# Optimization experiments

Hardware: AMD Instinct MI355X
Metric: run time of the kernel (lower is better)

Reference implementation:

```python
import jax, jax.numpy as jnp
import numpy as np

SR = 22050
L = 2097153            # output_size = int(SR*95.109); equals NFFT//2+1 so spectral broadcast is well-defined
NFFT = 4194304         # 2**ceil(log2(L))
BANDS = [(1.0, 4.0), (4.0, 8.0), (8.0, 13.0), (13.0, 30.0), (30.0, 100.0), (100.0, 200.0)]
SPEC = [7.83, 528.0, 396.0, 2.5, 14.1, 432.0, 6.0, 30.0]
WIN = 15               # min(15, NFFT//100)
FREQS_NP = np.fft.rfftfreq(NFFT, 1.0 / SR).astype(np.float32)
FREQS = jnp.asarray(FREQS_NP)


def _freq_mod(sig, band_w, freq_w, harm_prog, tm_w1, tm_b1, tm_w2, tm_b2, tm_w3, tm_b3):
    t = jnp.arange(L, dtype=jnp.float32)
    Xf = jnp.fft.rfft(jnp.pad(sig, (0, NFFT - L)))            # [L] complex64
    # sequential band enhancements == product of per-band multipliers
    mult = jnp.ones((L,), jnp.float32)
    for b, (lo, hi) in enumerate(BANDS):
        c = (lo + hi) / 2.0
        w = (hi - lo) / 2.0
        mask = jnp.exp(-0.5 * ((FREQS - c) / (w / 2.0)) ** 2)
        mask = jnp.where((FREQS < lo) | (FREQS > hi), 0.0, mask)
        tmod = jnp.sin(2.0 * np.pi * c * t / SR)
        mult = mult * (1.0 + mask * band_w[b] * (1.0 + 0.2 * tmod))
    # harmonic progression (identical for every specific frequency -> compute once)
    tn = (t / L)[:, None]
    h = jax.nn.relu(tn @ tm_w1 + tm_b1)
    h = jax.nn.relu(h @ tm_w2 + tm_b2)
    mp = h @ tm_w3 + tm_b3                                    # [L, 8]
    chord_idx = jnp.floor(t / L * 8.0).astype(jnp.int32) % 8
    chord = harm_prog[chord_idx] * (1.0 + mp[:, 1] * jnp.sin(2.0 * np.pi * t / L))[:, None]
    prog_mean = chord.mean()
    # specific-frequency harmonic windows (static indices; commutative multiplies)
    smult = jnp.ones((L,), jnp.float32)
    for k, f in enumerate(SPEC):
        for m in (1.0, 2.0, 3.0, 4.0, 5.0):
            hf = f * m
            if hf >= SR / 2:
                continue
            hidx = int(np.argmin(np.abs(FREQS_NP - hf)))
            s = max(0, hidx - WIN)
            e = min(L - 1, hidx + WIN)
            win = jnp.asarray(np.exp(-0.5 * ((np.arange(s, e + 1) - hidx) / (WIN / 3.0)) ** 2).astype(np.float32))
            enh = freq_w[k] * win * (1.0 / m ** 1.2) * (1.0 + prog_mean)
            smult = smult.at[s:e + 1].multiply(1.0 + enh)
    Xf = Xf * mult * smult
    mag = jnp.abs(Xf)
    ph = jnp.angle(Xf)
    mag_s = jnp.concatenate([mag[:1], mag[1:-1] * 0.7 + mag[:-2] * 0.15 + mag[2:] * 0.15, mag[-1:]])
    Xc = mag_s * jnp.exp(1j * ph)
    return jnp.fft.irfft(Xc, n=NFFT)[:L]


def _conv1d(x, w, b, stride):
    y = jax.lax.conv_general_dilated(x, w, (stride,), [(2, 2)], dimension_numbers=("NCH", "OIH", "NCH"))
    return y + b[None, :, None]


def setup_inputs() -> dict:
    key = jax.random.key(0)
    ks = jax.random.split(key, 16)
    n = lambda k, s, sc=1.0: jax.random.normal(k, s, dtype=jnp.float32) * sc
    return {
        "z": n(ks[0], (1, 1, L)),
        "condition": n(ks[1], (1, 8)),
        "band_w": jnp.full((6,), 0.5, jnp.float32),
        "freq_w": jnp.full((8,), 0.3, jnp.float32),
        "harm_prog": n(ks[2], (8, 4)),
        "tm_w1": n(ks[3], (1, 32), 0.5), "tm_b1": jnp.zeros((32,), jnp.float32),
        "tm_w2": n(ks[4], (32, 16), 0.2), "tm_b2": jnp.zeros((16,), jnp.float32),
        "tm_w3": n(ks[5], (16, 8), 0.2), "tm_b3": jnp.zeros((8,), jnp.float32),
        "c1_w": n(ks[6], (32, 1, 5), 0.3), "c1_b": jnp.zeros((32,), jnp.float32),
        "c2_w": n(ks[7], (64, 32, 5), 0.08), "c2_b": jnp.zeros((64,), jnp.float32),
        "c3_w": n(ks[8], (128, 64, 5), 0.05), "c3_b": jnp.zeros((128,), jnp.float32),
        "mx_w1": n(ks[9], (192, 256), 0.07), "mx_b1": jnp.zeros((256,), jnp.float32),
        "mx_w2": n(ks[10], (256, 1), 0.06), "mx_b2": jnp.zeros((1,), jnp.float32),
    }


def reference(z, condition, band_w, freq_w, harm_prog, tm_w1, tm_b1, tm_w2, tm_b2, tm_w3, tm_b3,
              c1_w, c1_b, c2_w, c2_b, c3_w, c3_b, mx_w1, mx_b1, mx_w2, mx_b2):
    base = _freq_mod(z[0, 0], band_w, freq_w, harm_prog, tm_w1, tm_b1, tm_w2, tm_b2, tm_w3, tm_b3)[None, None, :]
    h = jax.nn.leaky_relu(_conv1d(base, c1_w, c1_b, 2), 0.2)
    h = jax.nn.leaky_relu(_conv1d(h, c2_w, c2_b, 2), 0.2)
    h = jax.nn.leaky_relu(_conv1d(h, c3_w, c3_b, 2), 0.2)
    feat = h.mean(axis=2)                                     # [1, 128]
    emb = jnp.zeros((1, 64), jnp.float32)                     # instrument_idx=None path
    mixed = jnp.concatenate([feat, emb], axis=1)              # [1, 192]
    out = jax.nn.leaky_relu(mixed @ mx_w1 + mx_b1, 0.2) @ mx_w2 + mx_b2
    return out
```

## Files before the change

kernel.cpp:

```cpp
#include <hip/hip_runtime.h>
#include <cmath>

#define LSIG  2097153
#define MH    2097152
#define NFFTC 4194304
#define NT128 16384
#define O1C   1048577
#define O2C   524289
#define O3C   262145

#define TO3   62
#define NB3   4229

#define A_OFF    0
#define B_OFF    16777216
#define PM_OFF   58720268
#define FEAT_OFF 58720272
#define W2Q_OFF  50331664
#define W3Q_OFF  50352144
#define W1Q_OFF  50434064

struct SmultTab { int hidx[40]; float inv12[40]; int fk[40]; int maxe; };

typedef short short8 __attribute__((ext_vector_type(8)));
typedef float f32x4v __attribute__((ext_vector_type(4)));

union AFrag { uint4 q; short8 s; };
union BFrag { uint4 q; unsigned int u[4]; short8 s; };

__device__ __forceinline__ float lrelu(float a){ return a > 0.0f ? a : 0.2f*a; }

__device__ __forceinline__ float hsin(float rev){ return __builtin_amdgcn_sinf(rev); }
__device__ __forceinline__ float hcos(float rev){ return __builtin_amdgcn_cosf(rev); }

__device__ __forceinline__ unsigned int rbf(float f) {
  unsigned int u = __float_as_uint(f);
  u += 0x7fffu + ((u >> 16) & 1u);
  return u >> 16;
}
__device__ __forceinline__ unsigned int pack_bf2(float a, float b) {
  unsigned int r;
  asm("v_cvt_pk_bf16_f32 %0, %1, %2" : "=v"(r) : "v"(a), "v"(b));
  return r;
}

__device__ __forceinline__ int swz1(int pos, int dw) {
  return (pos*16 + dw) ^ (((pos >> 1) & 7) << 2);
}
__device__ __forceinline__ int swz2(int pos, int dw) {
  return (pos*32 + dw) ^ (((pos >> 1) & 7) << 2);
}

__device__ __forceinline__ int slot128(int jj, int q) {
  int s = q ^ ((q >> 4) & 7);
  return jj*128 + ((s + 9*jj) & 127);
}

__device__ __forceinline__ float2 cadd(float2 a, float2 b){ return make_float2(a.x+b.x, a.y+b.y); }
__device__ __forceinline__ float2 csub(float2 a, float2 b){ return make_float2(a.x-b.x, a.y-b.y); }

template<bool FWD> __device__ __forceinline__ float2 jrot(float2 z){
  return FWD ? make_float2(z.y, -z.x) : make_float2(-z.y, z.x);
}

template<bool FWD> __device__ __forceinline__ void dft8(float2 v[8]) {
  const float cq = 0.70710678118654752440f;
  const float S  = FWD ? -1.0f : 1.0f;
  float2 e0 = cadd(v[0], v[4]), e1 = csub(v[0], v[4]);
  float2 e2 = cadd(v[2], v[6]), e3 = csub(v[2], v[6]);
  float2 E0 = cadd(e0, e2), E2 = csub(e0, e2);
  float2 jt = jrot<FWD>(e3);
  float2 E1 = cadd(e1, jt), E3 = csub(e1, jt);
  float2 o0 = cadd(v[1], v[5]), o1 = csub(v[1], v[5]);
  float2 o2 = cadd(v[3], v[7]), o3 = csub(v[3], v[7]);
  float2 O0 = cadd(o0, o2), O2 = csub(o0, o2);
  float2 jo = jrot<FWD>(o3);
  float2 O1 = cadd(o1, jo), O3 = csub(o1, jo);
  float2 w1 = make_float2(cq*O1.x - S*cq*O1.y, cq*O1.y + S*cq*O1.x);
  float2 w2 = jrot<FWD>(O2);
  float2 w3 = make_float2(-cq*O3.x - S*cq*O3.y, -cq*O3.y + S*cq*O3.x);
  v[0] = cadd(E0, O0); v[4] = csub(E0, O0);
  v[1] = cadd(E1, w1); v[5] = csub(E1, w1);
  v[2] = cadd(E2, w2); v[6] = csub(E2, w2);
  v[3] = cadd(E3, w3); v[7] = csub(E3, w3);
}

template<bool FWD>
__device__ __forceinline__ void fft128_body(float2* stage, int t, int jb, int Ns) {
  const float ssg = FWD ? -1.0f : 1.0f;
  const float invden = 1.0f / (float)(128 * Ns);
  {
    const int jj = t >> 4, b = t & 15;
    const int m = (jb + jj) & (Ns - 1);
    float2 v[8];
#pragma unroll
    for (int a = 0; a < 8; ++a) {
      const int r = 16*a + b;
      float2 x = stage[slot128(jj, r)];
      if (Ns > 1) {
        float rev = (float)(m * r) * invden;
        float sn = ssg * hsin(rev), cs = hcos(rev);
        x = make_float2(x.x*cs - x.y*sn, x.x*sn + x.y*cs);
      }
      v[a] = x;
    }
    dft8<FWD>(v);
#pragma unroll
    for (int d = 0; d < 8; ++d)
      stage[slot128(jj, 16*d + b)] = v[d];
  }
  __syncthreads();
  {
    float2 y[16];
    const int jj = (t & 255) >> 3, d = t & 7;
    if (t < 256) {
#pragma unroll
      for (int b = 0; b < 16; ++b) {
        float2 x = stage[slot128(jj, 16*d + b)];
        float rev = (float)(b*d) * 0.0078125f;
        float sn = ssg * hsin(rev), cs = hcos(rev);
        y[b] = make_float2(x.x*cs - x.y*sn, x.x*sn + x.y*cs);
      }
    }
    __syncthreads();
    if (t < 256) {
      float2 E[8], O[8];
#pragma unroll
      for (int b = 0; b < 8; ++b) { E[b] = y[2*b]; O[b] = y[2*b+1]; }
      dft8<FWD>(E);
      dft8<FWD>(O);
#pragma unroll
      for (int c = 0; c < 8; ++c) {
        float rev = (float)c * 0.0625f;
        float sn = ssg * hsin(rev), cs = hcos(rev);
        float2 To = make_float2(O[c].x*cs - O[c].y*sn, O[c].x*sn + O[c].y*cs);
        stage[slot128(jj, 8*c + d)]      = cadd(E[c], To);
        stage[slot128(jj, 8*c + 64 + d)] = csub(E[c], To);
      }
    }
  }
  __syncthreads();
}

template<bool FWD, bool TRUNC>
__global__ __launch_bounds__(512) void kfft128(const float2* __restrict__ src,
                                               float2* __restrict__ dst, int Ns) {
  __shared__ float2 stage[4096];
  const int t = threadIdx.x;
  const int jb = blockIdx.x * 32;
  for (int c = 0; c < 4; ++c) {
    int u = t + 512*c;
    int jp = u & 15, rr = u >> 4;
    float4 q = *(const float4*)&src[jb + 2*jp + rr*NT128];
    stage[slot128(2*jp,   rr)] = make_float2(q.x, q.y);
    stage[slot128(2*jp+1, rr)] = make_float2(q.z, q.w);
  }
  __syncthreads();
  fft128_body<FWD>(stage, t, jb, Ns);
  if (Ns == 1) {
    for (int c = 0; c < 4; ++c) {
      int u = t + 512*c;
      int jj = u >> 6, k2 = (u & 63) * 2;
      float2 a = stage[slot128(jj, k2)], b = stage[slot128(jj, k2+1)];
      *(float4*)&dst[(jb + jj)*128 + k2] = make_float4(a.x, a.y, b.x, b.y);
    }
  } else {
    for (int c = 0; c < 4; ++c) {
      int u = t + 512*c;
      int pi = u & 15, k = u >> 4;
      int jj = 2*pi, j2 = jb + jj, m2 = j2 & (Ns - 1);
      int base = (j2 - m2)*128 + m2 + k*Ns;
      if (TRUNC && k >= 64) {
        if (k == 64 && j2 == 0) dst[base] = stage[slot128(jj, k)];
        continue;
      }
      float2 a = stage[slot128(jj, k)], b = stage[slot128(jj+1, k)];
      *(float4*)&dst[base] = make_float4(a.x, a.y, b.x, b.y);
    }
  }
}

__global__ __launch_bounds__(512) void kfirst(
    const float* __restrict__ zin, float2* __restrict__ dst,
    const float* __restrict__ tw1, const float* __restrict__ tb1,
    const float* __restrict__ tw2, const float* __restrict__ tb2,
    const float* __restrict__ tw3, const float* __restrict__ tb3,
    const float* __restrict__ hp, float* __restrict__ pm,
    float* __restrict__ feat) {
  __shared__ float2 stage[4096];
  __shared__ float shp[8];
  __shared__ float red[512];
  const int t = threadIdx.x;
  const int bb = blockIdx.x;
  if (bb < 512) {
    const int jb = bb * 32;
    for (int c = 0; c < 4; ++c) {
      int u = t + 512*c;
      int jp = u & 15, rr = u >> 4;
      int n = jb + 2*jp + rr*NT128;
      float2 a0, a1;
      if (n < 1048576) {
        float4 q = *(const float4*)&((const float2*)zin)[n];
        a0 = make_float2(q.x, q.y); a1 = make_float2(q.z, q.w);
      } else if (n == 1048576) {
        a0 = make_float2(zin[2097152], 0.0f); a1 = make_float2(0.0f, 0.0f);
      } else {
        a0 = make_float2(0.0f, 0.0f); a1 = a0;
      }
      stage[slot128(2*jp,   rr)] = a0;
      stage[slot128(2*jp+1, rr)] = a1;
    }
    __syncthreads();
    fft128_body<true>(stage, t, jb, 1);
    for (int c = 0; c < 4; ++c) {
      int u = t + 512*c;
      int jj = u >> 6, k2 = (u & 63) * 2;
      float2 a = stage[slot128(jj, k2)], b = stage[slot128(jj, k2+1)];
      *(float4*)&dst[(jb + jj)*128 + k2] = make_float4(a.x, a.y, b.x, b.y);
    }
    return;
  }
  if (t < 8) { float s = 0.f; for (int j = 0; j < 4; ++j) s += hp[t*4+j]; shp[t] = s; }
  __syncthreads();
  const int gid = (bb - 512)*512 + t;
  if (gid < 32768) feat[gid] = 0.0f;
  const float Lf = 2097153.0f;
  float tnv[4], sv[4];
  int ci[4];
  float acc[4][16];
#pragma unroll
  for (int e = 0; e < 4; ++e) {
    float ti = (float)(gid + e*524288);
    float tn = ti / Lf;
    tnv[e] = tn;
    sv[e] = hsin(tn);
    ci[e] = ((int)floorf(tn * 8.0f)) & 7;
#pragma unroll
    for (int kk = 0; kk < 16; ++kk) acc[e][kk] = tb2[kk];
  }
  for (int j = 0; j < 32; ++j) {
    float a = tw1[j], b = tb1[j];
    float hj[4];
#pragma unroll
    for (int e = 0; e < 4; ++e) hj[e] = fmaxf(a*tnv[e] + b, 0.0f);
#pragma unroll
    for (int kk = 0; kk < 16; ++kk) {
      float w = tw2[j*16 + kk];
#pragma unroll
      for (int e = 0; e < 4; ++e) acc[e][kk] += hj[e]*w;
    }
  }
  float lsum = 0.0f;
  const float b31 = tb3[1];
#pragma unroll
  for (int e = 0; e < 4; ++e) {
    float mp1 = b31;
#pragma unroll
    for (int kk = 0; kk < 16; ++kk) mp1 += fmaxf(acc[e][kk], 0.0f)*tw3[kk*8+1];
    lsum += shp[ci[e]] * (1.0f + mp1*sv[e]);
  }
  if (gid == 0) {
    float ti = 2097152.0f;
    float tn = ti / Lf;
    float a1[16];
    for (int kk = 0; kk < 16; ++kk) a1[kk] = tb2[kk];
    for (int j = 0; j < 32; ++j) {
      float h = fmaxf(tw1[j]*tn + tb1[j], 0.0f);
      for (int kk = 0; kk < 16; ++kk) a1[kk] += h*tw2[j*16+kk];
    }
    float mp1 = b31;
    for (int kk = 0; kk < 16; ++kk) mp1 += fmaxf(a1[kk], 0.0f)*tw3[kk*8+1];
    float svx = hsin(tn);
    int cix = ((int)floorf(tn * 8.0f)) & 7;
    lsum += shp[cix] * (1.0f + mp1*svx);
  }
  red[t] = lsum;
  __syncthreads();
  for (int off = 256; off > 0; off >>= 1) {
    if (t < off) red[t] += red[t+off];
    __syncthreads();
  }
  if (t == 0) atomicAdd(pm, red[0]);
}

__device__ __forceinline__ float2 xsplit(float2 zk, float2 zm, float rev) {
  float2 s  = make_float2(zk.x + zm.x, zk.y - zm.y);
  float2 dd = make_float2(zk.x - zm.x, zk.y + zm.y);
  float sn = -hsin(rev), cs = hcos(rev);
  float2 t1 = make_float2(cs*dd.x - sn*dd.y, cs*dd.y + sn*dd.x);
  return make_float2(0.5f*(s.x + t1.y), 0.5f*(s.y - t1.x));
}
__device__ __forceinline__ float2 scale_xc(float2 c, float mg, float ms) {
  if (mg > 0.0f) { float sc = ms/mg; return make_float2(c.x*sc, c.y*sc); }
  return make_float2(ms, 0.0f);
}
__device__ __forceinline__ float2 invpack(int n, float2 a, float2 b) {
  float2 s  = make_float2(a.x + b.x, a.y - b.y);
  float2 dd = make_float2(a.x - b.x, a.y + b.y);
  float rev = (float)n * (1.0f / (float)NFFTC);
  float sn = hsin(rev), cs = hcos(rev);
  float2 xo = make_float2(0.5f*(cs*dd.x - sn*dd.y), 0.5f*(cs*dd.y + sn*dd.x));
  const float sc = 1.0f / (float)MH;
  return make_float2((0.5f*s.x - xo.y)*sc, (0.5f*s.y + xo.x)*sc);
}

__global__ __launch_bounds__(256) void kspectral(const float2* __restrict__ Z,
    float2* __restrict__ A, const float* __restrict__ bwp,
    const float* __restrict__ fwp, const float* __restrict__ pm_in, SmultTab tab,
    const float* __restrict__ c1w, const float* __restrict__ c2w,
    const float* __restrict__ c3w, unsigned short* __restrict__ w1q,
    unsigned short* __restrict__ w2q, unsigned short* __restrict__ w3q) {
  const int bb = blockIdx.x;
  const int t = threadIdx.x;
  if (bb >= 4096) {
    int i = (bb - 4096)*256 + t;
    if (i < 1024) {
      int e = i & 7, u4 = i >> 3;
      int col = u4 & 15, quad = (u4 >> 4) & 3, mi = u4 >> 6;
      float v = (quad == 0 && e < 5) ? c1w[(mi*16 + col)*5 + e] : 0.0f;
      w1q[i] = (unsigned short)rbf(v);
    }
    if (i < 10240) {
      int e = i & 7, u4 = i >> 3;
      int col = u4 & 15, quad = (u4 >> 4) & 3, mtkt = u4 >> 6;
      int kt = mtkt % 5, mt = mtkt / 5;
      int ch = mt*16 + col, c1 = quad*8 + e;
      w2q[i] = (unsigned short)rbf(c2w[ch*160 + c1*5 + kt]);
    }
    if (i < 40960) {
      int e = i & 7, u4 = i >> 3;
      int col = u4 & 15, quad = (u4 >> 4) & 3, mtkt = u4 >> 6;
      int kt = mtkt % 10, mt = mtkt / 10;
      int ch = mt*16 + col, c2 = (kt & 1)*32 + quad*8 + e;
      w3q[i] = (unsigned short)rbf(c3w[ch*320 + c2*5 + (kt >> 1)]);
    }
    return;
  }
  __shared__ float2 Xlo[258], Xhi[258];
  __shared__ float  Mlo[258], Mhi[258];
  const int k0 = bb * 256;
  const float pm1 = 1.0f + pm_in[0] * (1.0f/8388612.0f);
  for (int w = t; w < 258; w += 256) {
    int k = k0 - 1 + w;
    float2 zk = Z[k & (MH-1)];
    float2 zm = Z[(MH - k) & (MH-1)];
    {
      float2 X = xsplit(zk, zm, (float)k * (1.0f/(float)NFFTC));
      float mv = 1.0f;
      if (k <= 38050) {
        const float blo[6] = {1.0f,4.0f,8.0f,13.0f,30.0f,100.0f};
        const float bhi[6] = {4.0f,8.0f,13.0f,30.0f,100.0f,200.0f};
        const float bcn[6] = {2.5f,6.0f,10.5f,21.5f,65.0f,150.0f};
        const float bhw[6] = {0.75f,1.0f,1.25f,4.25f,17.5f,25.0f};
        float f = (float)((double)k * (22050.0/4194304.0));
#pragma unroll
        for (int b = 0; b < 6; ++b) {
          if (f >= blo[b] && f <= bhi[b]) {
            float q = (f - bcn[b]) / bhw[b];
            float mask = expf(-0.5f*q*q);
            double frd = (double)k * ((double)bcn[b] / 22050.0);
            frd -= floor(frd);
            float tm = hsin((float)frd);
            mv *= (1.0f + mask * bwp[b] * (1.0f + 0.2f*tm));
          }
        }
      }
      if (k <= tab.maxe) {
        for (int ww = 0; ww < 40; ++ww) {
          int dlt = k - tab.hidx[ww];
          if (dlt >= -15 && dlt <= 15) {
            float x = (float)dlt * 0.2f;
            float win = expf(-0.5f*x*x);
            float enh = fwp[tab.fk[ww]] * win * tab.inv12[ww] * pm1;
            mv *= (1.0f + enh);
          }
        }
      }
      X.x *= mv; X.y *= mv;
      Xlo[w] = X; Mlo[w] = sqrtf(X.x*X.x + X.y*X.y);
    }
    {
      float2 X = xsplit(zm, zk, (float)(MH - k) * (1.0f/(float)NFFTC));
      Xhi[w] = X; Mhi[w] = sqrtf(X.x*X.x + X.y*X.y);
    }
  }
  __syncthreads();
  const int k = k0 + t, w = t + 1;
  float msl = (k == 0) ? Mlo[w] : 0.7f*Mlo[w] + 0.15f*(Mlo[w-1] + Mlo[w+1]);
  float2 xl = scale_xc(Xlo[w], Mlo[w], msl);
  float msh = (k == 0) ? Mhi[w] : 0.7f*Mhi[w] + 0.15f*(Mhi[w+1] + Mhi[w-1]);
  float2 xh = scale_xc(Xhi[w], Mhi[w], msh);
  A[k] = invpack(k, xl, xh);
  if (k >= 1) A[MH - k] = invpack(MH - k, xh, xl);
  if (bb == 4095 && t == 255) {
    float2 Xm = Xlo[257]; float Mm = Mlo[257];
    float ms = 0.7f*Mm + 0.15f*(Mlo[256] + Mhi[256]);
    float2 xm = scale_xc(Xm, Mm, ms);
    A[1048576] = invpack(1048576, xm, xm);
  }
}

__global__ __launch_bounds__(256, 4) void kconv(const float* __restrict__ x,
    const unsigned short* __restrict__ w1q, const unsigned short* __restrict__ w2q,
    const unsigned short* __restrict__ w3q, const float* __restrict__ c1b,
    const float* __restrict__ c2b, const float* __restrict__ c3b,
    float* __restrict__ feat) {
  __shared__ float sb[552];
  __shared__ unsigned int sh1[4352];
  __shared__ unsigned int sh2[4224];
  const int tid  = threadIdx.x;
  const int blk  = blockIdx.x;
  const int s3   = blk * TO3;
  const int lane = tid & 63;
  const int wv   = tid >> 6;
  const int col  = lane & 15;
  const int quad = lane >> 4;

  const uint4* W1 = (const uint4*)w1q;
  AFrag a1w[2];
#pragma unroll
  for (int mi = 0; mi < 2; ++mi)
    a1w[mi].q = W1[(mi*4 + quad)*16 + col];

  const uint4* W2 = (const uint4*)w2q;
  const int mt2 = (wv & 1) * 2;
  const int ntb2 = (wv >> 1) * 4;
  uint4 wk2[2][5];
#pragma unroll
  for (int mi = 0; mi < 2; ++mi)
#pragma unroll
    for (int kt = 0; kt < 5; ++kt)
      wk2[mi][kt] = W2[(((mt2+mi)*5 + kt)*4 + quad)*16 + col];

  float b1r[2][4], b2r[2][4];
#pragma unroll
  for (int mi = 0; mi < 2; ++mi)
#pragma unroll
    for (int r = 0; r < 4; ++r) {
      b1r[mi][r] = c1b[mi*16 + quad*4 + r];
      b2r[mi][r] = c2b[(mt2+mi)*16 + quad*4 + r];
    }

  {
    const int pb = 8*s3 - 14;
    for (int idx = tid; idx < 552; idx += 256) {
      int p = pb + idx;
      sb[idx] = (idx < 517 && p >= 0 && p < LSIG) ? x[p] : 0.0f;
    }
    if (tid < 128) sh2[4096 + tid] = 0u;
  }
  __syncthreads();

  {
    const int a1 = 4*s3 - 6;
    for (int nt = wv; nt < 17; nt += 4) {
      const int n = nt*16 + col;
      BFrag bf;
      if (quad == 0) {
        const float* ps = &sb[2*n];
        bf.u[0] = pack_bf2(ps[0], ps[1]);
        bf.u[1] = pack_bf2(ps[2], ps[3]);
        bf.u[2] = pack_bf2(ps[4], ps[5]);
        bf.u[3] = pack_bf2(ps[6], ps[7]);
      } else {
        bf.u[0] = 0u; bf.u[1] = 0u; bf.u[2] = 0u; bf.u[3] = 0u;
      }
      f32x4v acc[2];
      acc[0] = (f32x4v){b1r[0][0], b1r[0][1], b1r[0][2], b1r[0][3]};
      acc[1] = (f32x4v){b1r[1][0], b1r[1][1], b1r[1][2], b1r[1][3]};
      acc[0] = __builtin_amdgcn_mfma_f32_16x16x32_bf16(a1w[0].s, bf.s, acc[0], 0, 0, 0);
      acc[1] = __builtin_amdgcn_mfma_f32_16x16x32_bf16(a1w[1].s, bf.s, acc[1], 0, 0, 0);
      const int o1 = a1 + n;
      const bool ok = (n <= 257) && (o1 >= 0) && (o1 < O1C);
#pragma unroll
      for (int mi = 0; mi < 2; ++mi) {
        float v0 = ok ? lrelu(acc[mi][0]) : 0.0f;
        float v1 = ok ? lrelu(acc[mi][1]) : 0.0f;
        float v2 = ok ? lrelu(acc[mi][2]) : 0.0f;
        float v3 = ok ? lrelu(acc[mi][3]) : 0.0f;
        uint2 pk; pk.x = pack_bf2(v0, v1); pk.y = pack_bf2(v2, v3);
        *(uint2*)&sh1[swz1(n, mi*8 + quad*2)] = pk;
      }
    }
  }
  __syncthreads();

  f32x4v acc2[2][4];
#pragma unroll
  for (int mi = 0; mi < 2; ++mi)
#pragma unroll
    for (int nt = 0; nt < 4; ++nt)
      acc2[mi][nt] = (f32x4v){b2r[mi][0], b2r[mi][1], b2r[mi][2], b2r[mi][3]};
#pragma unroll
  for (int kt = 0; kt < 5; ++kt) {
#pragma unroll
    for (int nt = 0; nt < 4; ++nt) {
      const int n = (ntb2 + nt)*16 + col;
      const int row = 2*n + kt;
      BFrag bf;
      bf.q = *(const uint4*)&sh1[swz1(row, quad*4)];
      AFrag a0, a1; a0.q = wk2[0][kt]; a1.q = wk2[1][kt];
      acc2[0][nt] = __builtin_amdgcn_mfma_f32_16x16x32_bf16(a0.s, bf.s, acc2[0][nt], 0, 0, 0);
      acc2[1][nt] = __builtin_amdgcn_mfma_f32_16x16x32_bf16(a1.s, bf.s, acc2[1][nt], 0, 0, 0);
    }
  }

  {
    const int a2 = 2*s3 - 2;
#pragma unroll
    for (int nt = 0; nt < 4; ++nt) {
      const int p = (ntb2 + nt)*16 + col;
      const int o2 = a2 + p;
      const bool ok = (o2 >= 0) && (o2 < O2C);
#pragma unroll
      for (int mi = 0; mi < 2; ++mi) {
        float v0 = ok ? lrelu(acc2[mi][nt][0]) : 0.0f;
        float v1 = ok ? lrelu(acc2[mi][nt][1]) : 0.0f;
        float v2 = ok ? lrelu(acc2[mi][nt][2]) : 0.0f;
        float v3 = ok ? lrelu(acc2[mi][nt][3]) : 0.0f;
        const int dwb = (mt2+mi)*8 + quad*2;
        uint2 pk; pk.x = pack_bf2(v0, v1); pk.y = pack_bf2(v2, v3);
        *(uint2*)&sh2[swz2(p, dwb)] = pk;
      }
    }
  }
  __syncthreads();

  {
    const uint4* W3 = (const uint4*)w3q;
    const int slot = (blk & 255) * 128;
#pragma unroll
    for (int pass = 0; pass < 2; ++pass) {
      const int mt = wv + 4*pass;
      uint4 wk3[10];
#pragma unroll
      for (int kt = 0; kt < 10; ++kt)
        wk3[kt] = W3[((mt*10 + kt)*4 + quad)*16 + col];
      float b3r[4];
#pragma unroll
      for (int r = 0; r < 4; ++r) b3r[r] = c3b[mt*16 + quad*4 + r];
      f32x4v acc3[4];
#pragma unroll
      for (int nt = 0; nt < 4; ++nt)
        acc3[nt] = (f32x4v){b3r[0], b3r[1], b3r[2], b3r[3]};
#pragma unroll
      for (int kt = 0; kt < 10; ++kt) {
        const int tap = kt >> 1;
        const int hh  = (kt & 1) * 16;
#pragma unroll
        for (int nt = 0; nt < 4; ++nt) {
          const int n = nt*16 + col;
          const int row = 2*n + tap;
          BFrag bf;
          bf.q = *(const uint4*)&sh2[swz2(row, hh + quad*4)];
          AFrag a; a.q = wk3[kt];
          acc3[nt] = __builtin_amdgcn_mfma_f32_16x16x32_bf16(a.s, bf.s, acc3[nt], 0, 0, 0);
        }
      }
#pragma unroll
      for (int r = 0; r < 4; ++r) {
        const int ch = mt*16 + quad*4 + r;
        float v = 0.0f;
#pragma unroll
        for (int nt = 0; nt < 4; ++nt) {
          const int n = nt*16 + col;
          const bool ok = (n < TO3) && (s3 + n < O3C);
          if (ok) v += lrelu(acc3[nt][r]);
        }
        v += __shfl_xor(v, 1);
        v += __shfl_xor(v, 2);
        v += __shfl_xor(v, 4);
        v += __shfl_xor(v, 8);
        if (col == 0) atomicAdd(&feat[slot + ch], v);
      }
    }
  }
}

__global__ __launch_bounds__(256) void kfinal(const float* __restrict__ feat,
    const float* __restrict__ mw1, const float* __restrict__ mb1,
    const float* __restrict__ mw2, const float* __restrict__ mb2,
    float* __restrict__ out) {
  __shared__ float sfeat[128];
  __shared__ float red[256];
  const int tid = threadIdx.x;
  if (tid < 128) {
    float s = 0.0f;
    for (int sl = 0; sl < 256; ++sl) s += feat[sl*128 + tid];
    sfeat[tid] = s / 262145.0f;
  }
  __syncthreads();
  float y = mb1[tid];
  for (int i = 0; i < 128; ++i) y += sfeat[i] * mw1[i*256 + tid];
  y = y > 0.0f ? y : 0.2f*y;
  red[tid] = y * mw2[tid];
  __syncthreads();
  for (int off = 128; off > 0; off >>= 1) {
    if (tid < off) red[tid] += red[tid+off];
    __syncthreads();
  }
  if (tid == 0) out[0] = red[0] + mb2[0];
}

extern "C" void kernel_launch(void* const* d_in, const int* in_sizes, int n_in,
                              void* d_out, int out_size, void* d_ws, size_t ws_size,
                              hipStream_t stream) {
  (void)in_sizes; (void)n_in; (void)out_size; (void)ws_size;
  const float* z   = (const float*)d_in[0];
  const float* bw  = (const float*)d_in[2];
  const float* fw  = (const float*)d_in[3];
  const float* hp  = (const float*)d_in[4];
  const float* tw1 = (const float*)d_in[5];
  const float* tb1 = (const float*)d_in[6];
  const float* tw2 = (const float*)d_in[7];
  const float* tb2 = (const float*)d_in[8];
  const float* tw3 = (const float*)d_in[9];
  const float* tb3 = (const float*)d_in[10];
  const float* c1w = (const float*)d_in[11];
  const float* c1b = (const float*)d_in[12];
  const float* c2w = (const float*)d_in[13];
  const float* c2b = (const float*)d_in[14];
  const float* c3w = (const float*)d_in[15];
  const float* c3b = (const float*)d_in[16];
  const float* mw1 = (const float*)d_in[17];
  const float* mb1 = (const float*)d_in[18];
  const float* mw2 = (const float*)d_in[19];
  const float* mb2 = (const float*)d_in[20];

  char* wsb = (char*)d_ws;
  float2* A    = (float2*)(wsb + A_OFF);
  float2* B    = (float2*)(wsb + B_OFF);
  float*  PM   = (float*)(wsb + PM_OFF);
  float*  FEAT = (float*)(wsb + FEAT_OFF);
  unsigned short* W1Q = (unsigned short*)(wsb + W1Q_OFF);
  unsigned short* W2Q = (unsigned short*)(wsb + W2Q_OFF);
  unsigned short* W3Q = (unsigned short*)(wsb + W3Q_OFF);

  SmultTab tab;
  {
    const double spec[8] = {7.83, 528.0, 396.0, 2.5, 14.1, 432.0, 6.0, 30.0};
    int n = 0, maxe = 0;
    for (int kk = 0; kk < 8; ++kk)
      for (int m = 1; m <= 5; ++m) {
        double hf = spec[kk] * (double)m;
        if (hf >= 11025.0) continue;
        int hidx = (int)std::floor(hf * (4194304.0/22050.0) + 0.5);
        tab.hidx[n]  = hidx;
        tab.inv12[n] = (float)(1.0/std::pow((double)m, 1.2));
        tab.fk[n]    = kk;
        if (hidx + 15 > maxe) maxe = hidx + 15;
        ++n;
      }
    tab.maxe = maxe;
  }

  (void)hipMemsetAsync(wsb + PM_OFF, 0, 4, stream);

  kfirst<<<1536,512,0,stream>>>(z, A, tw1,tb1,tw2,tb2,tw3,tb3,hp, PM, FEAT);

  kfft128<true,false><<<512,512,0,stream>>>(A, B, 128);
  kfft128<true,false><<<512,512,0,stream>>>(B, A, 16384);

  kspectral<<<4256,256,0,stream>>>(A, B, bw, fw, PM, tab, c1w, c2w, c3w, W1Q, W2Q, W3Q);

  kfft128<false,false><<<512,512,0,stream>>>(B, A, 1);
  kfft128<false,false><<<512,512,0,stream>>>(A, B, 128);
  kfft128<false,true ><<<512,512,0,stream>>>(B, A, 16384);

  kconv<<<NB3,256,0,stream>>>((const float*)A, W1Q, W2Q, W3Q, c1b, c2b, c3b, FEAT);
  kfinal<<<1,256,0,stream>>>(FEAT, mw1, mb1, mw2, mb2, (float*)d_out);
}
```

Measured before the change: 254.7 us.

## Reassign conv2/conv3 MFMA work per wave to reuse B fragments across channel tiles

Conv2 now gives each wave all 4 output-channel tiles over 2 position tiles, so each LDS B-fragment read feeds 4 MFMAs instead of 2. Its weights and biases are loaded after conv1 and before the barrier, overlapping the global loads with the sync. Conv3 drops the two sequential passes: each wave handles 2 channel tiles at once, with weights loaded in two K halves, so each sh2 read feeds two MFMAs and the B reads are halved. The cost is more accumulator and weight registers live at once, which may lower occupancy or cause spills.

```diff
diff --git a/kernel.cpp b/kernel.cpp
--- a/kernel.cpp
+++ b/kernel.cpp
@@ -421,25 +421,12 @@
 #pragma unroll
   for (int mi = 0; mi < 2; ++mi)
     a1w[mi].q = W1[(mi*4 + quad)*16 + col];
-
-  const uint4* W2 = (const uint4*)w2q;
-  const int mt2 = (wv & 1) * 2;
-  const int ntb2 = (wv >> 1) * 4;
-  uint4 wk2[2][5];
+  float b1r[2][4];
 #pragma unroll
   for (int mi = 0; mi < 2; ++mi)
 #pragma unroll
-    for (int kt = 0; kt < 5; ++kt)
-      wk2[mi][kt] = W2[(((mt2+mi)*5 + kt)*4 + quad)*16 + col];
-
-  float b1r[2][4], b2r[2][4];
-#pragma unroll
-  for (int mi = 0; mi < 2; ++mi)
-#pragma unroll
-    for (int r = 0; r < 4; ++r) {
+    for (int r = 0; r < 4; ++r)
       b1r[mi][r] = c1b[mi*16 + quad*4 + r];
-      b2r[mi][r] = c2b[(mt2+mi)*16 + quad*4 + r];
-    }
 
   {
     const int pb = 8*s3 - 14;
@@ -483,42 +470,59 @@
       }
     }
   }
-  __syncthreads();
-
-  f32x4v acc2[2][4];
-#pragma unroll
-  for (int mi = 0; mi < 2; ++mi)
-#pragma unroll
-    for (int nt = 0; nt < 4; ++nt)
-      acc2[mi][nt] = (f32x4v){b2r[mi][0], b2r[mi][1], b2r[mi][2], b2r[mi][3]};
+
+  const uint4* W2 = (const uint4*)w2q;
+  uint4 wk2[4][5];
+#pragma unroll
+  for (int mt = 0; mt < 4; ++mt)
+#pragma unroll
+    for (int kt = 0; kt < 5; ++kt)
+      wk2[mt][kt] = W2[((mt*5 + kt)*4 + quad)*16 + col];
+  float b2r[4][4];
+#pragma unroll
+  for (int mt = 0; mt < 4; ++mt)
+#pragma unroll
+    for (int r = 0; r < 4; ++r)
+      b2r[mt][r] = c2b[mt*16 + quad*4 + r];
+  __syncthreads();
+
+  const int ntb2 = wv * 2;
+  f32x4v acc2[4][2];
+#pragma unroll
+  for (int mt = 0; mt < 4; ++mt)
+#pragma unroll
+    for (int nt = 0; nt < 2; ++nt)
+      acc2[mt][nt] = (f32x4v){b2r[mt][0], b2r[mt][1], b2r[mt][2], b2r[mt][3]};
 #pragma unroll
   for (int kt = 0; kt < 5; ++kt) {
 #pragma unroll
-    for (int nt = 0; nt < 4; ++nt) {
+    for (int nt = 0; nt < 2; ++nt) {
       const int n = (ntb2 + nt)*16 + col;
       const int row = 2*n + kt;
       BFrag bf;
       bf.q = *(const uint4*)&sh1[swz1(row, quad*4)];
-      AFrag a0, a1; a0.q = wk2[0][kt]; a1.q = wk2[1][kt];
-      acc2[0][nt] = __builtin_amdgcn_mfma_f32_16x16x32_bf16(a0.s, bf.s, acc2[0][nt], 0, 0, 0);
-      acc2[1][nt] = __builtin_amdgcn_mfma_f32_16x16x32_bf16(a1.s, bf.s, acc2[1][nt], 0, 0, 0);
+#pragma unroll
+      for (int mt = 0; mt < 4; ++mt) {
+        AFrag a; a.q = wk2[mt][kt];
+        acc2[mt][nt] = __builtin_amdgcn_mfma_f32_16x16x32_bf16(a.s, bf.s, acc2[mt][nt], 0, 0, 0);
+      }
     }
   }
 
   {
     const int a2 = 2*s3 - 2;
 #pragma unroll
-    for (int nt = 0; nt < 4; ++nt) {
+    for (int nt = 0; nt < 2; ++nt) {
       const int p = (ntb2 + nt)*16 + col;
       const int o2 = a2 + p;
       const bool ok = (o2 >= 0) && (o2 < O2C);
 #pragma unroll
-      for (int mi = 0; mi < 2; ++mi) {
-        float v0 = ok ? lrelu(acc2[mi][nt][0]) : 0.0f;
-        float v1 = ok ? lrelu(acc2[mi][nt][1]) : 0.0f;
-        float v2 = ok ? lrelu(acc2[mi][nt][2]) : 0.0f;
-        float v3 = ok ? lrelu(acc2[mi][nt][3]) : 0.0f;
-        const int dwb = (mt2+mi)*8 + quad*2;
+      for (int mt = 0; mt < 4; ++mt) {
+        float v0 = ok ? lrelu(acc2[mt][nt][0]) : 0.0f;
+        float v1 = ok ? lrelu(acc2[mt][nt][1]) : 0.0f;
+        float v2 = ok ? lrelu(acc2[mt][nt][2]) : 0.0f;
+        float v3 = ok ? lrelu(acc2[mt][nt][3]) : 0.0f;
+        const int dwb = mt*8 + quad*2;
         uint2 pk; pk.x = pack_bf2(v0, v1); pk.y = pack_bf2(v2, v3);
         *(uint2*)&sh2[swz2(p, dwb)] = pk;
       }
@@ -529,22 +533,35 @@
   {
     const uint4* W3 = (const uint4*)w3q;
     const int slot = (blk & 255) * 128;
-#pragma unroll
-    for (int pass = 0; pass < 2; ++pass) {
-      const int mt = wv + 4*pass;
-      uint4 wk3[10];
-#pragma unroll
-      for (int kt = 0; kt < 10; ++kt)
-        wk3[kt] = W3[((mt*10 + kt)*4 + quad)*16 + col];
-      float b3r[4];
-#pragma unroll
-      for (int r = 0; r < 4; ++r) b3r[r] = c3b[mt*16 + quad*4 + r];
-      f32x4v acc3[4];
-#pragma unroll
-      for (int nt = 0; nt < 4; ++nt)
-        acc3[nt] = (f32x4v){b3r[0], b3r[1], b3r[2], b3r[3]};
-#pragma unroll
-      for (int kt = 0; kt < 10; ++kt) {
+    const int mtb = wv * 2;
+    f32x4v acc3[2][4];
+#pragma unroll
+    for (int mi = 0; mi < 2; ++mi) {
+#pragma unroll
+      for (int r = 0; r < 4; ++r) {
+        float b3 = c3b[(mtb+mi)*16 + quad*4 + r];
+#pragma unroll
+        for (int nt = 0; nt < 4; ++nt) acc3[mi][nt][r] = (nt == 0) ? b3 : 0.0f;
+      }
+    }
+#pragma unroll
+    for (int mi = 0; mi < 2; ++mi)
+#pragma unroll
+      for (int nt = 1; nt < 4; ++nt)
+#pragma unroll
+        for (int r = 0; r < 4; ++r)
+          acc3[mi][nt][r] = acc3[mi][0][r];
+#pragma unroll
+    for (int kh = 0; kh < 2; ++kh) {
+      uint4 wk3[2][5];
+#pragma unroll
+      for (int mi = 0; mi < 2; ++mi)
+#pragma unroll
+        for (int kq = 0; kq < 5; ++kq)
+          wk3[mi][kq] = W3[(((mtb+mi)*10 + kh*5 + kq)*4 + quad)*16 + col];
+#pragma unroll
+      for (int kq = 0; kq < 5; ++kq) {
+        const int kt = kh*5 + kq;
         const int tap = kt >> 1;
         const int hh  = (kt & 1) * 16;
 #pragma unroll
@@ -553,19 +570,25 @@
           const int row = 2*n + tap;
           BFrag bf;
           bf.q = *(const uint4*)&sh2[swz2(row, hh + quad*4)];
-          AFrag a; a.q = wk3[kt];
-          acc3[nt] = __builtin_amdgcn_mfma_f32_16x16x32_bf16(a.s, bf.s, acc3[nt], 0, 0, 0);
+#pragma unroll
+          for (int mi = 0; mi < 2; ++mi) {
+            AFrag a; a.q = wk3[mi][kq];
+            acc3[mi][nt] = __builtin_amdgcn_mfma_f32_16x16x32_bf16(a.s, bf.s, acc3[mi][nt], 0, 0, 0);
+          }
         }
       }
+    }
+#pragma unroll
+    for (int mi = 0; mi < 2; ++mi) {
 #pragma unroll
       for (int r = 0; r < 4; ++r) {
-        const int ch = mt*16 + quad*4 + r;
+        const int ch = (mtb+mi)*16 + quad*4 + r;
         float v = 0.0f;
 #pragma unroll
         for (int nt = 0; nt < 4; ++nt) {
           const int n = nt*16 + col;
           const bool ok = (n < TO3) && (s3 + n < O3C);
-          if (ok) v += lrelu(acc3[nt][r]);
+          if (ok) v += lrelu(acc3[mi][nt][r]);
         }
         v += __shfl_xor(v, 1);
         v += __shfl_xor(v, 2);
```

After: 255.5 us. About the same (+0.3%).
